# Performance work log

Measured on AMD Instinct MI355X. Metric: run time of the kernel, lower is better.

## Reference

```python
import jax, jax.numpy as jnp
import numpy as np

B, T, D = 4, 2048, 2048
K, D_B, TOPK, WINDOW = 7, 128, 16, 64
GATE_CAP = 1.0
STRAND_CAP = 1.0
_PHI = 1.618033988749895
_PSI = -0.6180339887498949


def _ln(x, g, b, eps=1e-5):
    m = jnp.mean(x, axis=-1, keepdims=True)
    v = jnp.mean((x - m) ** 2, axis=-1, keepdims=True)
    return (x - m) * jax.lax.rsqrt(v + eps) * g + b


def setup_inputs() -> dict:
    ks = jax.random.split(jax.random.key(0), 20)
    rn = lambda k, s, sc=1.0: jax.random.normal(k, s, jnp.float32) * sc
    d_s = 1.0 / np.sqrt(D)
    db_s = 1.0 / np.sqrt(D_B)
    return {
        'X_write': rn(ks[0], (B, T, D)),
        'X_read': rn(ks[1], (B, T, D)),
        'slots': rn(ks[2], (B, K, D_B)),
        'W0': rn(ks[3], (D, D), d_s),
        'ln_write_g': jnp.ones((D,), jnp.float32),
        'ln_write_b': jnp.zeros((D,), jnp.float32),
        'Wv': rn(ks[4], (D_B, D), d_s),
        'Wk': rn(ks[5], (D_B, D_B), db_s),
        'slot_key_bias': rn(ks[6], (K, D_B), 2.0),
        'Wg_w': rn(ks[7], (D_B, 2 * D_B), 1.0 / np.sqrt(2 * D_B)),
        'Wg_b': jnp.full((D_B,), -2.0, jnp.float32),
        'ln_strand_g': jnp.ones((D_B,), jnp.float32),
        'ln_strand_b': jnp.zeros((D_B,), jnp.float32),
        'Wsq': rn(ks[8], (D_B, D_B), db_s),
        'Wsk': rn(ks[9], (D_B, D_B), db_s),
        'Wsv': rn(ks[10], (D_B, D_B), db_s),
        'lambda_strand': rn(ks[11], (D_B,), 0.1),
        'Wq_read': rn(ks[12], (D_B, D), d_s),
        'Wk_read': rn(ks[13], (D_B, D_B), db_s),
        'Wv_read': rn(ks[14], (D, D_B), db_s),
        'render_coeffs': rn(ks[15], (K, 3, D), 0.1),
        'slot_temps': 1.0 + rn(ks[16], (K,), 0.1),
    }


def reference(X_write, X_read, slots, W0, ln_write_g, ln_write_b, Wv, Wk,
              slot_key_bias, Wg_w, Wg_b, ln_strand_g, ln_strand_b,
              Wsq, Wsk, Wsv, lambda_strand, Wq_read, Wk_read, Wv_read,
              render_coeffs, slot_temps):
    b, t, d = X_write.shape
    sd = 1.0 / np.sqrt(D_B)
    X_n = _ln(X_write, ln_write_g, ln_write_b)

    # --- banded salience + topk (torch.no_grad region; only int indices escape) ---
    W_eff = min(WINDOW, t - 1)
    Xs = jax.lax.stop_gradient(X_n)
    X_W0 = Xs @ jax.lax.stop_gradient(W0).T            # [b,t,d]
    Xp = jnp.pad(X_W0, ((0, 0), (W_eff, 0), (0, 0)))   # left-pad so offset w -> j = i + w - W

    def band_dot(w):
        return jnp.einsum('btd,btd->bt', Xs,
                          jax.lax.dynamic_slice_in_dim(Xp, w, t, axis=1))

    band = jax.vmap(band_dot)(jnp.arange(W_eff)).transpose(1, 2, 0)  # [b,t,W]
    ii = jnp.arange(t)[:, None]
    ww = jnp.arange(W_eff)[None, :]
    jj = ii + ww - W_eff
    valid = (jj >= 0) & (ii >= 1)                      # j in [max(0,i-W), i)
    sal = jnp.where(valid, band, -jnp.inf).reshape(b, -1)
    topk_eff = min(TOPK, t * (t - 1) // 2)
    _, idx = jax.lax.top_k(sal, topk_eff)              # [b,topk]
    i_idx = idx // W_eff
    j_idx = i_idx + (idx % W_eff) - W_eff

    # --- topk pair gather + bilinear relation ---
    x_new = jnp.take_along_axis(X_n, i_idx[..., None], axis=1)  # [b,topk,d]
    x_old = jnp.take_along_axis(X_n, j_idx[..., None], axis=1)
    pair_sal = jnp.sum(x_new * (x_old @ jax.lax.stop_gradient(W0).T), axis=-1)
    alpha = jax.nn.softmax(pair_sal, axis=-1)
    R_t = jnp.einsum('bp,bpe->be', alpha, (x_new - x_old) @ Wv.T)  # [b,d_b]

    # --- slot write ---
    slot_keys = slots @ Wk.T + slot_key_bias[None]
    compat = jnp.einsum('bke,be->bk', slot_keys, R_t) * sd
    compat = compat * jax.nn.softplus(slot_temps)[None]
    sw = jax.nn.softmax(compat, axis=-1)
    weighted_R = sw[..., None] * R_t[:, None, :]                 # [b,K,d_b]
    g = jax.nn.sigmoid(jnp.concatenate([slots, weighted_R], -1) @ Wg_w.T + Wg_b)
    slots_upd = (1.0 - g) * slots + g * weighted_R

    # --- strand mixer (KxK self-attention) ---
    B_ln = _ln(slots_upd, ln_strand_g, ln_strand_b)
    att = jax.nn.softmax(jnp.einsum('bke,bme->bkm', B_ln @ Wsq.T, B_ln @ Wsk.T) * sd, axis=-1)
    ctx = att @ (B_ln @ Wsv.T)
    slots_next = slots_upd + ctx * jnp.clip(jnp.tanh(lambda_strand), -STRAND_CAP, STRAND_CAP)

    # --- aux losses ---
    L_persist = jnp.mean((slots_next - slots) ** 2)
    nrm = jnp.linalg.norm(slots_next, axis=-1, keepdims=True)
    Bn = slots_next / jnp.maximum(nrm, 1e-12)
    cos = jnp.einsum('bke,bme->bkm', Bn, Bn)
    off = 1.0 - jnp.eye(K, dtype=cos.dtype)
    L_div = jnp.sum(cos ** 2 * off) / (b * K * (K - 1))

    # --- directional render gate + read ---
    q_r = X_read @ Wq_read.T                    # [b,t,d_b]
    k_r = slots_next @ Wk_read.T                # [b,K,d_b]
    v_r = slots_next @ Wv_read.T                # [b,K,d]
    scores = jnp.einsum('bte,bke->btk', q_r, k_r) * sd
    q_mean = jnp.mean(X_read, axis=1)           # [b,d]
    w0q = q_mean @ jax.lax.stop_gradient(W0).T
    dphi = _PHI - _PSI
    phi_q = (w0q - _PSI * q_mean) / dphi
    psi_q = (_PHI * q_mean - w0q) / dphi
    pm = jnp.linalg.norm(phi_q, axis=-1, keepdims=True)
    sm = jnp.linalg.norm(psi_q, axis=-1, keepdims=True)
    tot = pm + sm + 1e-6
    basis = jnp.concatenate([jnp.ones_like(pm), pm / tot, sm / tot], axis=-1)  # [b,3]
    gate = jnp.clip(jnp.tanh(jnp.einsum('bi,kid->bkd', basis, render_coeffs)),
                    -GATE_CAP, GATE_CAP)
    z = jnp.einsum('btk,bkd->btd', jax.nn.softmax(scores, axis=-1), v_r * gate)
    return z, slots_next, L_persist, L_div
```

## Files before the change

### kernel.cpp

```cpp
#include <hip/hip_runtime.h>
#include <cstdint>
#include <cstddef>

#define DEV __device__ __forceinline__

typedef __bf16 bf16x8 __attribute__((ext_vector_type(8)));
typedef float f32x4 __attribute__((ext_vector_type(4)));
typedef unsigned short u16;
typedef unsigned int u32;

constexpr int Bq = 4, Tq = 2048, Dq = 2048, Kq = 7, DB = 128, TK = 16;
constexpr float SD = 0.08838834764831845f;
constexpr float PHIc = 1.618033988749895f;
constexpr float PSIc = -0.6180339887498949f;
constexpr float DPHI = 2.2360679774997896f;
#define NEG_INF (-__builtin_inff())

DEV u16 f2bf(float f) {
  union { float f; u32 u; } x; x.f = f;
  u32 r = (x.u + 0x7fffu + ((x.u >> 16) & 1u)) >> 16;
  return (u16)r;
}
DEV float bfbits2f(u32 h) { union { u32 u; float f; } x; x.u = h << 16; return x.f; }

DEV void async16(void* l, const void* g) {
  __builtin_amdgcn_global_load_lds((const __attribute__((address_space(1))) void*)g,
                                   (__attribute__((address_space(3))) void*)l, 16, 0, 0);
}

__global__ __launch_bounds__(256) void k_w0b(const float* __restrict__ W0, u16* __restrict__ W0b) {
  size_t i = ((size_t)blockIdx.x * 256 + threadIdx.x) * 8;
  float4 a = *(const float4*)&W0[i];
  float4 c = *(const float4*)&W0[i + 4];
  u32 p0 = (u32)f2bf(a.x) | ((u32)f2bf(a.y) << 16);
  u32 p1 = (u32)f2bf(a.z) | ((u32)f2bf(a.w) << 16);
  u32 p2 = (u32)f2bf(c.x) | ((u32)f2bf(c.y) << 16);
  u32 p3 = (u32)f2bf(c.z) | ((u32)f2bf(c.w) << 16);
  uint4 st; st.x = p0; st.y = p1; st.z = p2; st.w = p3;
  *(uint4*)&W0b[i] = st;
}

__global__ __launch_bounds__(256) void k_ln(const float* __restrict__ X, const float* __restrict__ g,
                                            const float* __restrict__ bb, u16* __restrict__ Xn) {
  int row = blockIdx.x;
  const float* xr = X + (size_t)row * Dq;
  int tid = threadIdx.x, lane = tid & 63, w = tid >> 6;
  float4 a = *(const float4*)&xr[tid * 8];
  float4 c = *(const float4*)&xr[tid * 8 + 4];
  float s = a.x + a.y + a.z + a.w + c.x + c.y + c.z + c.w;
  float q = a.x*a.x + a.y*a.y + a.z*a.z + a.w*a.w + c.x*c.x + c.y*c.y + c.z*c.z + c.w*c.w;
  #pragma unroll
  for (int o = 32; o; o >>= 1) { s += __shfl_xor(s, o); q += __shfl_xor(q, o); }
  __shared__ float red[8];
  if (lane == 0) { red[w] = s; red[w + 4] = q; }
  __syncthreads();
  float S = red[0] + red[1] + red[2] + red[3];
  float Q = red[4] + red[5] + red[6] + red[7];
  float mean = S * (1.0f / Dq);
  float var = Q * (1.0f / Dq) - mean * mean;
  float rstd = rsqrtf(var + 1e-5f);
  float v[8] = {a.x, a.y, a.z, a.w, c.x, c.y, c.z, c.w};
  u32 p[4];
  #pragma unroll
  for (int j = 0; j < 4; ++j) {
    int d0 = tid * 8 + j * 2;
    float o0 = (v[j*2]   - mean) * rstd * g[d0]   + bb[d0];
    float o1 = (v[j*2+1] - mean) * rstd * g[d0+1] + bb[d0+1];
    p[j] = (u32)f2bf(o0) | ((u32)f2bf(o1) << 16);
  }
  uint4 st; st.x = p[0]; st.y = p[1]; st.z = p[2]; st.w = p[3];
  *(uint4*)&Xn[(size_t)row * Dq + tid * 8] = st;
}

__global__ __launch_bounds__(256) void k_qmean1(const float* __restrict__ X, float* __restrict__ part) {
  int s = blockIdx.x;
  int y = blockIdx.y;
  int b = blockIdx.z;
  int tid = threadIdx.x;
  const float* xb = X + (size_t)b * Tq * Dq + (size_t)s * 1024 + tid * 4;
  f32x4 acc = {0.f, 0.f, 0.f, 0.f};
  #pragma unroll 4
  for (int t = 0; t < 64; ++t) {
    const float4 v = *(const float4*)&xb[(size_t)(y * 64 + t) * Dq];
    acc[0] += v.x; acc[1] += v.y; acc[2] += v.z; acc[3] += v.w;
  }
  float4 st; st.x = acc[0]; st.y = acc[1]; st.z = acc[2]; st.w = acc[3];
  *(float4*)&part[((size_t)(b * 32 + y)) * Dq + s * 1024 + tid * 4] = st;
}

__global__ __launch_bounds__(256) void k_qmean2(const float* __restrict__ part, float* __restrict__ qm) {
  int s = blockIdx.x, b = blockIdx.y, tid = threadIdx.x;
  int col = s * 1024 + tid * 4;
  f32x4 acc = {0.f, 0.f, 0.f, 0.f};
  #pragma unroll 8
  for (int y = 0; y < 32; ++y) {
    float4 v = *(const float4*)&part[((size_t)(b * 32 + y)) * Dq + col];
    acc[0] += v.x; acc[1] += v.y; acc[2] += v.z; acc[3] += v.w;
  }
  float4 st;
  st.x = acc[0] * (1.0f / Tq); st.y = acc[1] * (1.0f / Tq);
  st.z = acc[2] * (1.0f / Tq); st.w = acc[3] * (1.0f / Tq);
  *(float4*)&qm[(size_t)b * Dq + col] = st;
}

__global__ __launch_bounds__(256) void k_w0q(const float* __restrict__ W0, const float* __restrict__ qm,
                                             float* __restrict__ w0q) {
  __shared__ float qs[4][Dq];
  int tid = threadIdx.x, lane = tid & 63, w = tid >> 6;
  for (int i = tid * 4; i < 4 * Dq; i += 1024) {
    *(float4*)&((float*)qs)[i] = *(const float4*)&qm[i];
  }
  __syncthreads();
  #pragma unroll
  for (int r = 0; r < 8; ++r) {
    int d = blockIdx.x * 32 + w * 8 + r;
    const float* wr = W0 + (size_t)d * Dq;
    float a0 = 0, a1 = 0, a2 = 0, a3 = 0;
    for (int e = lane * 4; e < Dq; e += 256) {
      float4 wv = *(const float4*)&wr[e];
      float4 q0 = *(const float4*)&qs[0][e];
      float4 q1 = *(const float4*)&qs[1][e];
      float4 q2 = *(const float4*)&qs[2][e];
      float4 q3 = *(const float4*)&qs[3][e];
      a0 += wv.x*q0.x + wv.y*q0.y + wv.z*q0.z + wv.w*q0.w;
      a1 += wv.x*q1.x + wv.y*q1.y + wv.z*q1.z + wv.w*q1.w;
      a2 += wv.x*q2.x + wv.y*q2.y + wv.z*q2.z + wv.w*q2.w;
      a3 += wv.x*q3.x + wv.y*q3.y + wv.z*q3.z + wv.w*q3.w;
    }
    #pragma unroll
    for (int o = 32; o; o >>= 1) {
      a0 += __shfl_xor(a0, o); a1 += __shfl_xor(a1, o);
      a2 += __shfl_xor(a2, o); a3 += __shfl_xor(a3, o);
    }
    if (lane == 0) {
      w0q[0 * Dq + d] = a0; w0q[1 * Dq + d] = a1;
      w0q[2 * Dq + d] = a2; w0q[3 * Dq + d] = a3;
    }
  }
}

__global__ __launch_bounds__(256) void k_basis(const float* __restrict__ qm, const float* __restrict__ w0q,
                                               float* __restrict__ basis) {
  int tid = threadIdx.x;
  __shared__ float red[256];
  __shared__ float psum;
  for (int b = 0; b < 4; ++b) {
    float ps = 0, ss = 0;
    for (int d = tid; d < Dq; d += 256) {
      float qv = qm[b * Dq + d], wv = w0q[b * Dq + d];
      float ph = (wv - PSIc * qv) * (1.0f / DPHI);
      float pv = (PHIc * qv - wv) * (1.0f / DPHI);
      ps += ph * ph; ss += pv * pv;
    }
    red[tid] = ps; __syncthreads();
    for (int st = 128; st; st >>= 1) { if (tid < st) red[tid] += red[tid + st]; __syncthreads(); }
    if (tid == 0) psum = red[0];
    __syncthreads();
    red[tid] = ss; __syncthreads();
    for (int st = 128; st; st >>= 1) { if (tid < st) red[tid] += red[tid + st]; __syncthreads(); }
    if (tid == 0) {
      float pm = sqrtf(psum), sm = sqrtf(red[0]);
      float tot = pm + sm + 1e-6f;
      basis[b * 3 + 0] = 1.0f; basis[b * 3 + 1] = pm / tot; basis[b * 3 + 2] = sm / tot;
    }
    __syncthreads();
  }
}

__global__ __launch_bounds__(256) void k_gemm(const u16* __restrict__ A, const u16* __restrict__ B,
                                              u16* __restrict__ C, int M, int N, int K) {
  __shared__ u16 As[128 * 64], Bs[128 * 64];
  int tid = threadIdx.x, lane = tid & 63, w = tid >> 6, wr = w >> 1, wc = w & 1;
  int bm = blockIdx.x, bn = blockIdx.y;
  const u16* Ab = A + (size_t)bm * 128 * K;
  const u16* Bb = B + (size_t)bn * 128 * K;
  f32x4 zero = {0.f, 0.f, 0.f, 0.f};
  f32x4 acc[4][4];
  #pragma unroll
  for (int mi = 0; mi < 4; ++mi)
    #pragma unroll
    for (int ni = 0; ni < 4; ++ni) acc[mi][ni] = zero;
  int ro = tid >> 3;
  int co = (tid & 7) * 8;
  int cs = co ^ ((ro & 7) * 8);
  for (int k0 = 0; k0 < K; k0 += 64) {
    #pragma unroll
    for (int i = 0; i < 4; ++i) {
      int row = ro + i * 32;
      async16(&As[row * 64 + co], Ab + (size_t)row * K + k0 + cs);
      async16(&Bs[row * 64 + co], Bb + (size_t)row * K + k0 + cs);
    }
    __syncthreads();
    #pragma unroll
    for (int ks = 0; ks < 2; ++ks) {
      int cbase = ks * 32 + ((lane >> 4) * 8);
      int crd = cbase ^ ((lane & 7) * 8);
      bf16x8 af[4], bfr[4];
      #pragma unroll
      for (int mi = 0; mi < 4; ++mi)
        af[mi] = *(const bf16x8*)&As[(wr * 64 + mi * 16 + (lane & 15)) * 64 + crd];
      #pragma unroll
      for (int ni = 0; ni < 4; ++ni)
        bfr[ni] = *(const bf16x8*)&Bs[(wc * 64 + ni * 16 + (lane & 15)) * 64 + crd];
      #pragma unroll
      for (int mi = 0; mi < 4; ++mi)
        #pragma unroll
        for (int ni = 0; ni < 4; ++ni)
          acc[mi][ni] = __builtin_amdgcn_mfma_f32_16x16x32_bf16(af[mi], bfr[ni], acc[mi][ni], 0, 0, 0);
    }
    __syncthreads();
  }
  int r0 = bm * 128 + wr * 64, c0 = bn * 128 + wc * 64;
  #pragma unroll
  for (int mi = 0; mi < 4; ++mi)
    #pragma unroll
    for (int ni = 0; ni < 4; ++ni) {
      int col = c0 + ni * 16 + (lane & 15);
      int rb = r0 + mi * 16 + ((lane >> 4) * 4);
      #pragma unroll
      for (int rg = 0; rg < 4; ++rg)
        C[(size_t)(rb + rg) * N + col] = f2bf(acc[mi][ni][rg]);
    }
}

__global__ __launch_bounds__(768) void k_band(const u16* __restrict__ Xn, const u16* __restrict__ XW0,
                                              float* __restrict__ sal) {
  int b = blockIdx.y, i0 = blockIdx.x * 32;
  int tid = threadIdx.x, lane = tid & 63, w = tid >> 6;
  int mi = w / 6, ni = w % 6;
  const u16* Xb = Xn + (size_t)b * Tq * Dq;
  const u16* Wb = XW0 + (size_t)b * Tq * Dq;
  int koff = (lane >> 4) * 8;
  const u16* ap = Xb + (size_t)(i0 + mi * 16 + (lane & 15)) * Dq + koff;
  int j = i0 - 64 + ni * 16 + (lane & 15); j = min(max(j, 0), Tq - 1);
  const u16* bp = Wb + (size_t)j * Dq + koff;
  f32x4 zero = {0.f, 0.f, 0.f, 0.f};
  f32x4 accA = zero, accB = zero;
  for (int k = 0; k < Dq; k += 64) {
    bf16x8 a0 = *(const bf16x8*)(ap + k);
    bf16x8 b0 = *(const bf16x8*)(bp + k);
    bf16x8 a1 = *(const bf16x8*)(ap + k + 32);
    bf16x8 b1 = *(const bf16x8*)(bp + k + 32);
    accA = __builtin_amdgcn_mfma_f32_16x16x32_bf16(a0, b0, accA, 0, 0, 0);
    accB = __builtin_amdgcn_mfma_f32_16x16x32_bf16(a1, b1, accB, 0, 0, 0);
  }
  int nl = ni * 16 + (lane & 15);
  #pragma unroll
  for (int rg = 0; rg < 4; ++rg) {
    int i = i0 + mi * 16 + (lane >> 4) * 4 + rg;
    int wb = nl - (i - i0);
    if (wb >= 0 && wb < 64) {
      int jj = i0 - 64 + nl;
      bool valid = (jj >= 0) && (i >= 1);
      sal[((size_t)b * Tq + i) * 64 + wb] = valid ? (accA[rg] + accB[rg]) : NEG_INF;
    }
  }
}

__global__ __launch_bounds__(256) void k_topk1(const float* __restrict__ sal,
                                               float* __restrict__ cv, int* __restrict__ ci) {
  int b = blockIdx.y, chunk = blockIdx.x;
  int tid = threadIdx.x, lane = tid & 63;
  const float* s = sal + (size_t)b * Tq * 64 + (size_t)chunk * 1024;
  float lv[4]; int li[4];
  #pragma unroll
  for (int i = 0; i < 4; ++i) { lv[i] = NEG_INF; li[i] = -1; }
  #pragma unroll
  for (int i = 0; i < 4; ++i) {
    int e = tid + i * 256;
    float v = s[e];
    int idx = chunk * 1024 + e;
    if (v > lv[3]) {
      lv[3] = v; li[3] = idx;
      #pragma unroll
      for (int q = 3; q > 0; --q)
        if (lv[q] > lv[q - 1]) {
          float tv = lv[q]; lv[q] = lv[q - 1]; lv[q - 1] = tv;
          int t2 = li[q]; li[q] = li[q - 1]; li[q - 1] = t2;
        }
    }
  }
  __shared__ float Sv[256][4];
  __shared__ int Si[256][4];
  __shared__ int heads[256];
  #pragma unroll
  for (int i = 0; i < 4; ++i) { Sv[tid][i] = lv[i]; Si[tid][i] = li[i]; }
  heads[tid] = 0;
  __syncthreads();
  float* ov = cv + ((size_t)b * 128 + chunk) * 16;
  int* oi = ci + ((size_t)b * 128 + chunk) * 16;
  for (int r = 0; r < 16; ++r) {
    if (tid < 64) {
      float best = NEG_INF; int bl = 0; int bidx = 0x7fffffff;
      #pragma unroll
      for (int cc = 0; cc < 4; ++cc) {
        int c = lane + cc * 64;
        int h = heads[c];
        float v = (h < 4) ? Sv[c][h] : NEG_INF;
        int ix = (h < 4) ? Si[c][h] : 0x7fffffff;
        if (v > best || (v == best && ix < bidx)) { best = v; bl = c; bidx = ix; }
      }
      #pragma unroll
      for (int o = 32; o; o >>= 1) {
        float bv = __shfl_xor(best, o); int blx = __shfl_xor(bl, o); int bix = __shfl_xor(bidx, o);
        if (bv > best || (bv == best && bix < bidx)) { best = bv; bl = blx; bidx = bix; }
      }
      if (lane == 0) {
        int h = heads[bl];
        ov[r] = best; oi[r] = (h < 4) ? Si[bl][h] : -1;
        heads[bl] = h + 1;
      }
    }
    __syncthreads();
  }
}

__global__ __launch_bounds__(256) void k_topk2(const float* __restrict__ cv, const int* __restrict__ ci,
                                               int* __restrict__ ti, int* __restrict__ tj) {
  int b = blockIdx.x, tid = threadIdx.x, lane = tid & 63;
  __shared__ float Sv[128][16];
  __shared__ int Si[128][16];
  __shared__ int heads[128];
  __shared__ int ridx[16];
  for (int i = tid; i < 128 * 16; i += 256) {
    ((float*)Sv)[i] = cv[(size_t)b * 2048 + i];
    ((int*)Si)[i] = ci[(size_t)b * 2048 + i];
  }
  if (tid < 128) heads[tid] = 0;
  __syncthreads();
  for (int r = 0; r < 16; ++r) {
    if (tid < 64) {
      float best = NEG_INF; int bl = 0; int bidx = 0x7fffffff;
      #pragma unroll
      for (int cc = 0; cc < 2; ++cc) {
        int c = lane + cc * 64;
        int h = heads[c];
        float v = (h < 16) ? Sv[c][h] : NEG_INF;
        int ix = (h < 16) ? Si[c][h] : 0x7fffffff;
        if (v > best || (v == best && ix < bidx)) { best = v; bl = c; bidx = ix; }
      }
      #pragma unroll
      for (int o = 32; o; o >>= 1) {
        float bv = __shfl_xor(best, o); int blx = __shfl_xor(bl, o); int bix = __shfl_xor(bidx, o);
        if (bv > best || (bv == best && bix < bidx)) { best = bv; bl = blx; bidx = bix; }
      }
      if (lane == 0) {
        int h = heads[bl];
        ridx[r] = Si[bl][h];
        heads[bl] = h + 1;
      }
    }
    __syncthreads();
  }
  if (tid < 16) {
    int fi = ridx[tid];
    int ii = fi >> 6;
    int jj = ii + (fi & 63) - 64;
    ti[b * TK + tid] = ii;
    tj[b * TK + tid] = jj;
  }
}

__global__ __launch_bounds__(256) void k_gatherln(const float* __restrict__ X, const float* __restrict__ g,
    const float* __restrict__ bb, const int* __restrict__ ti, const int* __restrict__ tj,
    float* __restrict__ Xnew, float* __restrict__ Xold) {
  int b = blockIdx.y, p = blockIdx.x >> 1, side = blockIdx.x & 1;
  int row = side ? tj[b * TK + p] : ti[b * TK + p];
  row = min(max(row, 0), Tq - 1);
  const float* xr = X + ((size_t)(b * Tq + row)) * Dq;
  float* dst = (side ? Xold : Xnew) + ((size_t)(b * TK + p)) * Dq;
  int tid = threadIdx.x, lane = tid & 63, w = tid >> 6;
  float4 a = *(const float4*)&xr[tid * 8];
  float4 c = *(const float4*)&xr[tid * 8 + 4];
  float s = a.x + a.y + a.z + a.w + c.x + c.y + c.z + c.w;
  float q = a.x*a.x + a.y*a.y + a.z*a.z + a.w*a.w + c.x*c.x + c.y*c.y + c.z*c.z + c.w*c.w;
  #pragma unroll
  for (int o = 32; o; o >>= 1) { s += __shfl_xor(s, o); q += __shfl_xor(q, o); }
  __shared__ float red[8];
  if (lane == 0) { red[w] = s; red[w + 4] = q; }
  __syncthreads();
  float S = red[0] + red[1] + red[2] + red[3];
  float Q = red[4] + red[5] + red[6] + red[7];
  float mean = S * (1.0f / Dq);
  float var = Q * (1.0f / Dq) - mean * mean;
  float rstd = rsqrtf(var + 1e-5f);
  float v[8] = {a.x, a.y, a.z, a.w, c.x, c.y, c.z, c.w};
  float o8[8];
  #pragma unroll
  for (int j = 0; j < 8; ++j) {
    int d = tid * 8 + j;
    o8[j] = (v[j] - mean) * rstd * g[d] + bb[d];
  }
  float4 s0; s0.x = o8[0]; s0.y = o8[1]; s0.z = o8[2]; s0.w = o8[3];
  float4 s1; s1.x = o8[4]; s1.y = o8[5]; s1.z = o8[6]; s1.w = o8[7];
  *(float4*)&dst[tid * 8] = s0;
  *(float4*)&dst[tid * 8 + 4] = s1;
}

__global__ __launch_bounds__(256) void k_pairsal(const float* __restrict__ W0, const float* __restrict__ Xnew,
                                                 const float* __restrict__ Xold, float* __restrict__ psal) {
  int d0 = blockIdx.x * 64, e0 = blockIdx.y * 64;
  int tid = threadIdx.x, P = tid & 63, dg = tid >> 6;
  f32x4 xo[16];
  #pragma unroll
  for (int i = 0; i < 16; ++i)
    xo[i] = *(const f32x4*)&Xold[(size_t)P * Dq + e0 + i * 4];
  int dbase = d0 + dg * 16;
  f32x4 xn[4];
  #pragma unroll
  for (int i = 0; i < 4; ++i)
    xn[i] = *(const f32x4*)&Xnew[(size_t)P * Dq + dbase + i * 4];
  float acc = 0.f;
  #pragma unroll
  for (int dd = 0; dd < 16; ++dd) {
    int d = __builtin_amdgcn_readfirstlane(dbase + dd);
    const float* wr = W0 + (size_t)d * Dq + e0;
    float i0 = 0.f, i1 = 0.f, i2 = 0.f, i3 = 0.f;
    #pragma unroll
    for (int i = 0; i < 16; ++i) {
      float4 wv = *(const float4*)&wr[i * 4];
      i0 += wv.x * xo[i][0]; i1 += wv.y * xo[i][1];
      i2 += wv.z * xo[i][2]; i3 += wv.w * xo[i][3];
    }
    acc += xn[dd >> 2][dd & 3] * ((i0 + i1) + (i2 + i3));
  }
  __shared__ float part[4][64];
  part[dg][P] = acc;
  __syncthreads();
  if (tid < 64)
    atomicAdd(&psal[tid], part[0][tid] + part[1][tid] + part[2][tid] + part[3][tid]);
}

__global__ __launch_bounds__(256) void k_alphart(const float* __restrict__ psal, const float* __restrict__ Xnew,
    const float* __restrict__ Xold, const float* __restrict__ Wv, float* __restrict__ Rt) {
  int bx = blockIdx.x, b = blockIdx.y;
  int tid = threadIdx.x, lane = tid & 63, w = tid >> 6;
  __shared__ float al[16], xd[Dq];
  if (tid == 0) {
    float mx = NEG_INF;
    #pragma unroll
    for (int p = 0; p < 16; ++p) mx = fmaxf(mx, psal[b * 16 + p]);
    float ee[16]; float s = 0.f;
    #pragma unroll
    for (int p = 0; p < 16; ++p) { ee[p] = expf(psal[b * 16 + p] - mx); s += ee[p]; }
    #pragma unroll
    for (int p = 0; p < 16; ++p) al[p] = ee[p] / s;
  }
  __syncthreads();
  {
    int d0 = tid * 8;
    float a8[8] = {0, 0, 0, 0, 0, 0, 0, 0};
    #pragma unroll
    for (int p = 0; p < 16; ++p) {
      const float* xn = Xnew + (size_t)(b * 16 + p) * Dq + d0;
      const float* xo = Xold + (size_t)(b * 16 + p) * Dq + d0;
      float ap = al[p];
      float4 n0 = *(const float4*)xn;
      float4 n1 = *(const float4*)(xn + 4);
      float4 o0 = *(const float4*)xo;
      float4 o1 = *(const float4*)(xo + 4);
      a8[0] += ap * (n0.x - o0.x); a8[1] += ap * (n0.y - o0.y);
      a8[2] += ap * (n0.z - o0.z); a8[3] += ap * (n0.w - o0.w);
      a8[4] += ap * (n1.x - o1.x); a8[5] += ap * (n1.y - o1.y);
      a8[6] += ap * (n1.z - o1.z); a8[7] += ap * (n1.w - o1.w);
    }
    #pragma unroll
    for (int j = 0; j < 8; ++j) xd[d0 + j] = a8[j];
  }
  __syncthreads();
  int e = bx * 4 + w;
  const float* wr = Wv + (size_t)e * Dq;
  float s = 0.f;
  #pragma unroll 8
  for (int d = lane; d < Dq; d += 64) s += wr[d] * xd[d];
  #pragma unroll
  for (int o = 32; o; o >>= 1) s += __shfl_xor(s, o);
  if (lane == 0) Rt[b * DB + e] = s;
}

__global__ __launch_bounds__(1024) void k_slots(
    const float* __restrict__ slots, const float* __restrict__ Wk, const float* __restrict__ skb,
    const float* __restrict__ Wgw, const float* __restrict__ Wgb,
    const float* __restrict__ lng, const float* __restrict__ lnb,
    const float* __restrict__ Wsq, const float* __restrict__ Wsk, const float* __restrict__ Wsv,
    const float* __restrict__ lam, const float* __restrict__ temps,
    const float* __restrict__ Rt, const float* __restrict__ Wkr,
    float* __restrict__ snOut, float* __restrict__ krOut) {
  int b = blockIdx.x, tid = threadIdx.x;
  int lane = tid & 63, w = tid >> 6;
  int sub = lane & 15, quad = lane >> 4;
  __shared__ float s_s[Kq][DB], r_s[DB], sk_s[Kq][DB], cm[8], sw[8],
                   su[Kq][DB], mv[Kq][2], bnl[Kq][DB],
                   qq[Kq][DB], kks[Kq][DB], vvs[Kq][DB],
                   att[Kq][8], sn_s[Kq][DB];
  for (int i = tid; i < Kq * DB; i += 1024) ((float*)s_s)[i] = slots[(size_t)b * Kq * DB + i];
  if (tid < DB) r_s[tid] = Rt[b * DB + tid];
  __syncthreads();
  #pragma unroll
  for (int r = 0; r < 14; ++r) {
    int idx = (w * 14 + r) * 4 + quad;
    int k = idx >> 7, e = idx & 127;
    const float* wr = Wk + e * DB;
    float a = 0.f;
    #pragma unroll
    for (int j = 0; j < 8; ++j) a += wr[sub + j * 16] * s_s[k][sub + j * 16];
    a += __shfl_xor(a, 8); a += __shfl_xor(a, 4); a += __shfl_xor(a, 2); a += __shfl_xor(a, 1);
    if (sub == 0) sk_s[k][e] = a + skb[idx];
  }
  __syncthreads();
  if (w < Kq) {
    float a = sk_s[w][lane] * r_s[lane] + sk_s[w][lane + 64] * r_s[lane + 64];
    #pragma unroll
    for (int o = 32; o; o >>= 1) a += __shfl_xor(a, o);
    if (lane == 0) {
      float t = temps[w];
      cm[w] = a * SD * log1pf(expf(t));
    }
  }
  __syncthreads();
  if (tid == 0) {
    float mx = cm[0];
    for (int k = 1; k < Kq; ++k) mx = fmaxf(mx, cm[k]);
    float ee[7]; float s = 0.f;
    for (int k = 0; k < Kq; ++k) { ee[k] = expf(cm[k] - mx); s += ee[k]; }
    for (int k = 0; k < Kq; ++k) sw[k] = ee[k] / s;
  }
  __syncthreads();
  #pragma unroll
  for (int r = 0; r < 14; ++r) {
    int idx = (w * 14 + r) * 4 + quad;
    int k = idx >> 7, e = idx & 127;
    const float* wr = Wgw + e * 256;
    float swk = sw[k];
    float a = 0.f;
    #pragma unroll
    for (int j = 0; j < 16; ++j) {
      int col = sub + j * 16;
      float x = (j < 8) ? s_s[k][col] : swk * r_s[col - 128];
      a += wr[col] * x;
    }
    a += __shfl_xor(a, 8); a += __shfl_xor(a, 4); a += __shfl_xor(a, 2); a += __shfl_xor(a, 1);
    if (sub == 0) {
      a += Wgb[e];
      float gv = 1.0f / (1.0f + expf(-a));
      float wrv = swk * r_s[e];
      su[k][e] = (1.0f - gv) * s_s[k][e] + gv * wrv;
    }
  }
  __syncthreads();
  if (w < Kq) {
    float v0 = su[w][lane], v1 = su[w][lane + 64];
    float s = v0 + v1, q = v0 * v0 + v1 * v1;
    #pragma unroll
    for (int o = 32; o; o >>= 1) { s += __shfl_xor(s, o); q += __shfl_xor(q, o); }
    if (lane == 0) {
      float m = s / DB; float va = q / DB - m * m;
      mv[w][0] = m; mv[w][1] = rsqrtf(va + 1e-5f);
    }
  }
  __syncthreads();
  for (int i = tid; i < Kq * DB; i += 1024) {
    int k = i >> 7, e = i & 127;
    bnl[k][e] = (su[k][e] - mv[k][0]) * mv[k][1] * lng[e] + lnb[e];
  }
  __syncthreads();
  #pragma unroll
  for (int r = 0; r < 14; ++r) {
    int idx = (w * 14 + r) * 4 + quad;
    int k = idx >> 7, e = idx & 127;
    const float* wr1 = Wsq + e * DB;
    const float* wr2 = Wsk + e * DB;
    const float* wr3 = Wsv + e * DB;
    float a1 = 0.f, a2 = 0.f, a3 = 0.f;
    #pragma unroll
    for (int j = 0; j < 8; ++j) {
      float x = bnl[k][sub + j * 16];
      a1 += wr1[sub + j * 16] * x;
      a2 += wr2[sub + j * 16] * x;
      a3 += wr3[sub + j * 16] * x;
    }
    #pragma unroll
    for (int o = 8; o; o >>= 1) {
      a1 += __shfl_xor(a1, o); a2 += __shfl_xor(a2, o); a3 += __shfl_xor(a3, o);
    }
    if (sub == 0) { qq[k][e] = a1; kks[k][e] = a2; vvs[k][e] = a3; }
  }
  __syncthreads();
  {
    int t4 = w * 4 + quad;
    if (t4 < 49) {
      int k = t4 / 7, m = t4 % 7;
      float a = 0.f;
      #pragma unroll
      for (int j = 0; j < 8; ++j) a += qq[k][sub + j * 16] * kks[m][sub + j * 16];
      a += __shfl_xor(a, 8); a += __shfl_xor(a, 4); a += __shfl_xor(a, 2); a += __shfl_xor(a, 1);
      if (sub == 0) att[k][m] = a * SD;
    }
  }
  __syncthreads();
  if (tid < Kq) {
    float mx = att[tid][0];
    for (int m = 1; m < Kq; ++m) mx = fmaxf(mx, att[tid][m]);
    float ee[7]; float s = 0.f;
    for (int m = 0; m < Kq; ++m) { ee[m] = expf(att[tid][m] - mx); s += ee[m]; }
    for (int m = 0; m < Kq; ++m) att[tid][m] = ee[m] / s;
  }
  __syncthreads();
  for (int i = tid; i < Kq * DB; i += 1024) {
    int k = i >> 7, e = i & 127;
    float c = 0.f;
    #pragma unroll
    for (int m = 0; m < Kq; ++m) c += att[k][m] * vvs[m][e];
    float l = tanhf(lam[e]); l = fminf(fmaxf(l, -1.0f), 1.0f);
    float v = su[k][e] + c * l;
    sn_s[k][e] = v;
    snOut[(size_t)b * Kq * DB + i] = v;
  }
  __syncthreads();
  #pragma unroll
  for (int r = 0; r < 14; ++r) {
    int idx = (w * 14 + r) * 4 + quad;
    int k = idx >> 7, e = idx & 127;
    const float* wr = Wkr + e * DB;
    float a = 0.f;
    #pragma unroll
    for (int j = 0; j < 8; ++j) a += wr[sub + j * 16] * sn_s[k][sub + j * 16];
    a += __shfl_xor(a, 8); a += __shfl_xor(a, 4); a += __shfl_xor(a, 2); a += __shfl_xor(a, 1);
    if (sub == 0) krOut[(size_t)b * Kq * DB + idx] = a;
  }
}

__global__ __launch_bounds__(256) void k_mvg(const float* __restrict__ snOut, const float* __restrict__ krOut,
    const float* __restrict__ Wqr, const float* __restrict__ Wvr, const float* __restrict__ rc,
    const float* __restrict__ basis, u16* __restrict__ Mb, u16* __restrict__ Vgb) {
  int b = blockIdx.y, tid = threadIdx.x;
  int d = blockIdx.x * 256 + tid;
  __shared__ float krs[Kq][DB], sns[Kq][DB];
  for (int i = tid; i < Kq * DB; i += 256) {
    ((float*)krs)[i] = krOut[(size_t)b * Kq * DB + i];
    ((float*)sns)[i] = snOut[(size_t)b * Kq * DB + i];
  }
  __syncthreads();
  float b0 = basis[b * 3 + 0], b1 = basis[b * 3 + 1], b2 = basis[b * 3 + 2];
  float am[7] = {0, 0, 0, 0, 0, 0, 0};
  for (int e = 0; e < DB; ++e) {
    float wq = Wqr[(size_t)e * Dq + d];
    #pragma unroll
    for (int k = 0; k < 7; ++k) am[k] += krs[k][e] * wq;
  }
  float vr[7] = {0, 0, 0, 0, 0, 0, 0};
  const float* wvrow = Wvr + (size_t)d * DB;
  for (int e = 0; e < DB; ++e) {
    float wv = wvrow[e];
    #pragma unroll
    for (int k = 0; k < 7; ++k) vr[k] += sns[k][e] * wv;
  }
  #pragma unroll
  for (int k = 0; k < 7; ++k) {
    Mb[((size_t)b * 7 + k) * Dq + d] = f2bf(am[k]);
    float gt = tanhf(b0 * rc[((size_t)k * 3 + 0) * Dq + d] +
                     b1 * rc[((size_t)k * 3 + 1) * Dq + d] +
                     b2 * rc[((size_t)k * 3 + 2) * Dq + d]);
    gt = fminf(fmaxf(gt, -1.0f), 1.0f);
    Vgb[((size_t)b * 7 + k) * Dq + d] = f2bf(vr[k] * gt);
  }
}

__global__ __launch_bounds__(256) void k_losses(const float* __restrict__ slots, const float* __restrict__ sn,
                                                float* __restrict__ out2) {
  int tid = threadIdx.x;
  __shared__ float red[256];
  __shared__ float nrm[28];
  float p = 0.f;
  for (int i = tid; i < Bq * Kq * DB; i += 256) { float d = sn[i] - slots[i]; p += d * d; }
  red[tid] = p; __syncthreads();
  for (int st = 128; st; st >>= 1) { if (tid < st) red[tid] += red[tid + st]; __syncthreads(); }
  if (tid == 0) out2[0] = red[0] / (float)(Bq * Kq * DB);
  if (tid < 28) {
    int b = tid / 7, k = tid % 7;
    float s = 0.f;
    for (int e = 0; e < DB; ++e) { float v = sn[(size_t)(b * 7 + k) * DB + e]; s += v * v; }
    nrm[tid] = fmaxf(sqrtf(s), 1e-12f);
  }
  __syncthreads();
  float dv = 0.f;
  if (tid < 168) {
    int b = tid / 42, r = tid % 42;
    int k = r / 6, m = r % 6; m += (m >= k);
    float dot = 0.f;
    for (int e = 0; e < DB; ++e)
      dot += sn[(size_t)(b * 7 + k) * DB + e] * sn[(size_t)(b * 7 + m) * DB + e];
    float c = dot / (nrm[b * 7 + k] * nrm[b * 7 + m]);
    dv = c * c;
  }
  red[tid] = dv; __syncthreads();
  for (int st = 128; st; st >>= 1) { if (tid < st) red[tid] += red[tid + st]; __syncthreads(); }
  if (tid == 0) out2[1] = red[0] / 168.0f;
}

__global__ __launch_bounds__(256) void k_z(const float* __restrict__ X, const u16* __restrict__ Mb,
                                           const u16* __restrict__ Vgb, float* __restrict__ Z) {
  int b = blockIdx.y, t0 = blockIdx.x * 16;
  int tid = threadIdx.x, lane = tid & 63, w = tid >> 6;
  __shared__ u16 Ms[7 * 2048], Vs[7 * 2048];
  for (int i = tid * 4; i < 7 * 2048; i += 1024) {
    *(uint2*)&Ms[i] = *(const uint2*)&Mb[(size_t)b * 7 * 2048 + i];
    *(uint2*)&Vs[i] = *(const uint2*)&Vgb[(size_t)b * 7 * 2048 + i];
  }
  __syncthreads();
  for (int ri = 0; ri < 4; ++ri) {
    int t = t0 + ri * 4 + w;
    const float* xr = X + ((size_t)b * Tq + t) * Dq;
    float sc[7] = {0, 0, 0, 0, 0, 0, 0};
    #pragma unroll
    for (int i = 0; i < 8; ++i) {
      int d = lane * 4 + i * 256;
      float4 x = *(const float4*)&xr[d];
      #pragma unroll
      for (int k = 0; k < 7; ++k) {
        uint2 mm = *(const uint2*)&Ms[k * 2048 + d];
        sc[k] += x.x * bfbits2f(mm.x & 0xffffu) + x.y * bfbits2f(mm.x >> 16)
               + x.z * bfbits2f(mm.y & 0xffffu) + x.w * bfbits2f(mm.y >> 16);
      }
    }
    #pragma unroll
    for (int k = 0; k < 7; ++k) {
      #pragma unroll
      for (int o = 32; o; o >>= 1) sc[k] += __shfl_xor(sc[k], o);
    }
    float mx = sc[0];
    #pragma unroll
    for (int k = 1; k < 7; ++k) mx = fmaxf(mx, sc[k]);
    float pz[7]; float s = 0.f;
    #pragma unroll
    for (int k = 0; k < 7; ++k) { pz[k] = expf((sc[k] - mx) * SD); s += pz[k]; }
    float inv = 1.0f / s;
    #pragma unroll
    for (int k = 0; k < 7; ++k) pz[k] *= inv;
    float* zr = Z + ((size_t)b * Tq + t) * Dq;
    #pragma unroll
    for (int i = 0; i < 8; ++i) {
      int d = lane * 4 + i * 256;
      float4 o4; o4.x = o4.y = o4.z = o4.w = 0.f;
      #pragma unroll
      for (int k = 0; k < 7; ++k) {
        uint2 vm = *(const uint2*)&Vs[k * 2048 + d];
        float pk = pz[k];
        o4.x += pk * bfbits2f(vm.x & 0xffffu); o4.y += pk * bfbits2f(vm.x >> 16);
        o4.z += pk * bfbits2f(vm.y & 0xffffu); o4.w += pk * bfbits2f(vm.y >> 16);
      }
      *(float4*)&zr[d] = o4;
    }
  }
}

extern "C" void kernel_launch(void* const* d_in, const int* in_sizes, int n_in,
                              void* d_out, int out_size, void* d_ws, size_t ws_size,
                              hipStream_t stream) {
  const float* Xw   = (const float*)d_in[0];
  const float* Xr   = (const float*)d_in[1];
  const float* slots= (const float*)d_in[2];
  const float* W0   = (const float*)d_in[3];
  const float* lng  = (const float*)d_in[4];
  const float* lnb  = (const float*)d_in[5];
  const float* Wv   = (const float*)d_in[6];
  const float* Wk   = (const float*)d_in[7];
  const float* skb  = (const float*)d_in[8];
  const float* Wgw  = (const float*)d_in[9];
  const float* Wgb  = (const float*)d_in[10];
  const float* lsg  = (const float*)d_in[11];
  const float* lsb  = (const float*)d_in[12];
  const float* Wsq  = (const float*)d_in[13];
  const float* Wsk  = (const float*)d_in[14];
  const float* Wsv  = (const float*)d_in[15];
  const float* lam  = (const float*)d_in[16];
  const float* Wqr  = (const float*)d_in[17];
  const float* Wkr  = (const float*)d_in[18];
  const float* Wvr  = (const float*)d_in[19];
  const float* rc   = (const float*)d_in[20];
  const float* temps= (const float*)d_in[21];

  char* wsb = (char*)d_ws;
  size_t off = 0;
  auto alloc = [&](size_t bytes) -> void* {
    void* p = wsb + off;
    off += (bytes + 255) & ~(size_t)255;
    return p;
  };
  u16*   Xn   = (u16*)  alloc((size_t)Bq * Tq * Dq * 2);
  u16*   XW0  = (u16*)  alloc((size_t)Bq * Tq * Dq * 2);
  u16*   W0b  = (u16*)  alloc((size_t)Dq * Dq * 2);
  float* sal  = (float*)alloc((size_t)Bq * Tq * 64 * 4);
  int*   ti   = (int*)  alloc(Bq * TK * 4);
  int*   tj   = (int*)  alloc(Bq * TK * 4);
  float* Xnew = (float*)alloc((size_t)Bq * TK * Dq * 4);
  float* Xold = (float*)alloc((size_t)Bq * TK * Dq * 4);
  float* psal = (float*)alloc(Bq * TK * 4);
  float* Rt   = (float*)alloc(Bq * DB * 4);
  float* qm   = (float*)alloc(Bq * Dq * 4);
  float* w0q  = (float*)alloc(Bq * Dq * 4);
  float* basis= (float*)alloc(Bq * 3 * 4);
  float* krOut= (float*)alloc(Bq * Kq * DB * 4);
  u16*   Mbf  = (u16*)  alloc((size_t)Bq * Kq * Dq * 2);
  u16*   Vgb  = (u16*)  alloc((size_t)Bq * Kq * Dq * 2);
  float* cv   = (float*)alloc((size_t)Bq * 128 * 16 * 4);
  int*   ci   = (int*)  alloc((size_t)Bq * 128 * 16 * 4);
  float* part = (float*)alloc((size_t)Bq * 32 * Dq * 4);

  float* Zout = (float*)d_out;
  float* snOut = Zout + (size_t)Bq * Tq * Dq;
  float* lossOut = snOut + Bq * Kq * DB;

  k_w0b   <<<2048, 256, 0, stream>>>(W0, W0b);
  k_ln    <<<Bq * Tq, 256, 0, stream>>>(Xw, lng, lnb, Xn);
  k_qmean1<<<dim3(2, 32, Bq), 256, 0, stream>>>(Xr, part);
  k_qmean2<<<dim3(2, Bq), 256, 0, stream>>>(part, qm);
  k_w0q   <<<64, 256, 0, stream>>>(W0, qm, w0q);
  k_basis <<<1, 256, 0, stream>>>(qm, w0q, basis);
  k_gemm  <<<dim3(64, 16), 256, 0, stream>>>(Xn, W0b, XW0, Bq * Tq, Dq, Dq);
  k_band  <<<dim3(64, Bq), 768, 0, stream>>>(Xn, XW0, sal);
  k_topk1 <<<dim3(128, Bq), 256, 0, stream>>>(sal, cv, ci);
  k_topk2 <<<Bq, 256, 0, stream>>>(cv, ci, ti, tj);
  k_gatherln<<<dim3(32, Bq), 256, 0, stream>>>(Xw, lng, lnb, ti, tj, Xnew, Xold);
  hipMemsetAsync(psal, 0, Bq * TK * 4, stream);
  k_pairsal<<<dim3(32, 32), 256, 0, stream>>>(W0, Xnew, Xold, psal);
  k_alphart<<<dim3(32, Bq), 256, 0, stream>>>(psal, Xnew, Xold, Wv, Rt);
  k_slots <<<Bq, 1024, 0, stream>>>(slots, Wk, skb, Wgw, Wgb, lsg, lsb, Wsq, Wsk, Wsv,
                                    lam, temps, Rt, Wkr, snOut, krOut);
  k_mvg   <<<dim3(8, Bq), 256, 0, stream>>>(snOut, krOut, Wqr, Wvr, rc, basis, Mbf, Vgb);
  k_losses<<<1, 256, 0, stream>>>(slots, snOut, lossOut);
  k_z     <<<dim3(128, Bq), 256, 0, stream>>>(Xr, Mbf, Vgb, Zout);
}
```

Baseline: 444.9 us.

## Split slot update into per-slot kernels and widen small reduction grids

Replaces the single per-batch 1024-thread slot-update kernel with four kernels gridded over (slot, batch), passing intermediates through global buffers so more CUs work on the tiny slot math. k_w0q is launched with 256 blocks of 2 rows per wave instead of 64 blocks, and k_basis runs one block per batch instead of looping over batches. k_z now reads the M/V tables directly from global memory instead of staging them in shared memory. These small kernels are latency-bound, so the extra launches and global round trips may cancel the parallelism gain, and dropping the LDS staging in k_z relies on cache hits.

```diff
diff --git a/kernel.cpp b/kernel.cpp
--- a/kernel.cpp
+++ b/kernel.cpp
@@ -73,9 +73,7 @@
 }
 
 __global__ __launch_bounds__(256) void k_qmean1(const float* __restrict__ X, float* __restrict__ part) {
-  int s = blockIdx.x;
-  int y = blockIdx.y;
-  int b = blockIdx.z;
+  int s = blockIdx.x, y = blockIdx.y, b = blockIdx.z;
   int tid = threadIdx.x;
   const float* xb = X + (size_t)b * Tq * Dq + (size_t)s * 1024 + tid * 4;
   f32x4 acc = {0.f, 0.f, 0.f, 0.f};
@@ -112,8 +110,8 @@
   }
   __syncthreads();
   #pragma unroll
-  for (int r = 0; r < 8; ++r) {
-    int d = blockIdx.x * 32 + w * 8 + r;
+  for (int r = 0; r < 2; ++r) {
+    int d = blockIdx.x * 8 + w * 2 + r;
     const float* wr = W0 + (size_t)d * Dq;
     float a0 = 0, a1 = 0, a2 = 0, a3 = 0;
     for (int e = lane * 4; e < Dq; e += 256) {
@@ -141,29 +139,26 @@
 
 __global__ __launch_bounds__(256) void k_basis(const float* __restrict__ qm, const float* __restrict__ w0q,
                                                float* __restrict__ basis) {
-  int tid = threadIdx.x;
+  int b = blockIdx.x, tid = threadIdx.x;
   __shared__ float red[256];
   __shared__ float psum;
-  for (int b = 0; b < 4; ++b) {
-    float ps = 0, ss = 0;
-    for (int d = tid; d < Dq; d += 256) {
-      float qv = qm[b * Dq + d], wv = w0q[b * Dq + d];
-      float ph = (wv - PSIc * qv) * (1.0f / DPHI);
-      float pv = (PHIc * qv - wv) * (1.0f / DPHI);
-      ps += ph * ph; ss += pv * pv;
-    }
-    red[tid] = ps; __syncthreads();
-    for (int st = 128; st; st >>= 1) { if (tid < st) red[tid] += red[tid + st]; __syncthreads(); }
-    if (tid == 0) psum = red[0];
-    __syncthreads();
-    red[tid] = ss; __syncthreads();
-    for (int st = 128; st; st >>= 1) { if (tid < st) red[tid] += red[tid + st]; __syncthreads(); }
-    if (tid == 0) {
-      float pm = sqrtf(psum), sm = sqrtf(red[0]);
-      float tot = pm + sm + 1e-6f;
-      basis[b * 3 + 0] = 1.0f; basis[b * 3 + 1] = pm / tot; basis[b * 3 + 2] = sm / tot;
-    }
-    __syncthreads();
+  float ps = 0, ss = 0;
+  for (int d = tid; d < Dq; d += 256) {
+    float qv = qm[b * Dq + d], wv = w0q[b * Dq + d];
+    float ph = (wv - PSIc * qv) * (1.0f / DPHI);
+    float pv = (PHIc * qv - wv) * (1.0f / DPHI);
+    ps += ph * ph; ss += pv * pv;
+  }
+  red[tid] = ps; __syncthreads();
+  for (int st = 128; st; st >>= 1) { if (tid < st) red[tid] += red[tid + st]; __syncthreads(); }
+  if (tid == 0) psum = red[0];
+  __syncthreads();
+  red[tid] = ss; __syncthreads();
+  for (int st = 128; st; st >>= 1) { if (tid < st) red[tid] += red[tid + st]; __syncthreads(); }
+  if (tid == 0) {
+    float pm = sqrtf(psum), sm = sqrtf(red[0]);
+    float tot = pm + sm + 1e-6f;
+    basis[b * 3 + 0] = 1.0f; basis[b * 3 + 1] = pm / tot; basis[b * 3 + 2] = sm / tot;
   }
 }
 
@@ -478,65 +473,70 @@
   if (lane == 0) Rt[b * DB + e] = s;
 }
 
-__global__ __launch_bounds__(1024) void k_slots(
-    const float* __restrict__ slots, const float* __restrict__ Wk, const float* __restrict__ skb,
-    const float* __restrict__ Wgw, const float* __restrict__ Wgb,
+__global__ __launch_bounds__(256) void ksl_a(const float* __restrict__ slots, const float* __restrict__ Wk,
+    const float* __restrict__ skb, const float* __restrict__ Rt, const float* __restrict__ temps,
+    float* __restrict__ compat) {
+  int k = blockIdx.x, b = blockIdx.y;
+  int tid = threadIdx.x, g = tid >> 4, sub = tid & 15;
+  __shared__ float s_s[DB], r_s[DB], sk_s[DB];
+  if (tid < DB) { s_s[tid] = slots[((size_t)(b * Kq + k)) * DB + tid]; r_s[tid] = Rt[b * DB + tid]; }
+  __syncthreads();
+  #pragma unroll
+  for (int r = 0; r < 8; ++r) {
+    int e = g * 8 + r;
+    const float* wr = Wk + e * DB;
+    float a = 0.f;
+    #pragma unroll
+    for (int j = 0; j < 8; ++j) a += wr[sub + j * 16] * s_s[sub + j * 16];
+    a += __shfl_xor(a, 8); a += __shfl_xor(a, 4); a += __shfl_xor(a, 2); a += __shfl_xor(a, 1);
+    if (sub == 0) sk_s[e] = a + skb[k * DB + e];
+  }
+  __syncthreads();
+  if (tid < 64) {
+    float a = sk_s[tid] * r_s[tid] + sk_s[tid + 64] * r_s[tid + 64];
+    #pragma unroll
+    for (int o = 32; o; o >>= 1) a += __shfl_xor(a, o);
+    if (tid == 0) {
+      float t = temps[k];
+      compat[b * Kq + k] = a * SD * log1pf(expf(t));
+    }
+  }
+}
+
+__global__ __launch_bounds__(64) void ksl_b(const float* __restrict__ compat, float* __restrict__ swg) {
+  int b = blockIdx.x;
+  if (threadIdx.x == 0) {
+    float cm[Kq];
+    float mx = NEG_INF;
+    for (int k = 0; k < Kq; ++k) { cm[k] = compat[b * Kq + k]; mx = fmaxf(mx, cm[k]); }
+    float s = 0.f;
+    for (int k = 0; k < Kq; ++k) { cm[k] = expf(cm[k] - mx); s += cm[k]; }
+    for (int k = 0; k < Kq; ++k) swg[b * Kq + k] = cm[k] / s;
+  }
+}
+
+__global__ __launch_bounds__(256) void ksl_c(const float* __restrict__ slots, const float* __restrict__ Rt,
+    const float* __restrict__ swg, const float* __restrict__ Wgw, const float* __restrict__ Wgb,
     const float* __restrict__ lng, const float* __restrict__ lnb,
     const float* __restrict__ Wsq, const float* __restrict__ Wsk, const float* __restrict__ Wsv,
-    const float* __restrict__ lam, const float* __restrict__ temps,
-    const float* __restrict__ Rt, const float* __restrict__ Wkr,
-    float* __restrict__ snOut, float* __restrict__ krOut) {
-  int b = blockIdx.x, tid = threadIdx.x;
-  int lane = tid & 63, w = tid >> 6;
-  int sub = lane & 15, quad = lane >> 4;
-  __shared__ float s_s[Kq][DB], r_s[DB], sk_s[Kq][DB], cm[8], sw[8],
-                   su[Kq][DB], mv[Kq][2], bnl[Kq][DB],
-                   qq[Kq][DB], kks[Kq][DB], vvs[Kq][DB],
-                   att[Kq][8], sn_s[Kq][DB];
-  for (int i = tid; i < Kq * DB; i += 1024) ((float*)s_s)[i] = slots[(size_t)b * Kq * DB + i];
-  if (tid < DB) r_s[tid] = Rt[b * DB + tid];
-  __syncthreads();
-  #pragma unroll
-  for (int r = 0; r < 14; ++r) {
-    int idx = (w * 14 + r) * 4 + quad;
-    int k = idx >> 7, e = idx & 127;
-    const float* wr = Wk + e * DB;
-    float a = 0.f;
-    #pragma unroll
-    for (int j = 0; j < 8; ++j) a += wr[sub + j * 16] * s_s[k][sub + j * 16];
-    a += __shfl_xor(a, 8); a += __shfl_xor(a, 4); a += __shfl_xor(a, 2); a += __shfl_xor(a, 1);
-    if (sub == 0) sk_s[k][e] = a + skb[idx];
-  }
-  __syncthreads();
-  if (w < Kq) {
-    float a = sk_s[w][lane] * r_s[lane] + sk_s[w][lane + 64] * r_s[lane + 64];
-    #pragma unroll
-    for (int o = 32; o; o >>= 1) a += __shfl_xor(a, o);
-    if (lane == 0) {
-      float t = temps[w];
-      cm[w] = a * SD * log1pf(expf(t));
-    }
-  }
-  __syncthreads();
-  if (tid == 0) {
-    float mx = cm[0];
-    for (int k = 1; k < Kq; ++k) mx = fmaxf(mx, cm[k]);
-    float ee[7]; float s = 0.f;
-    for (int k = 0; k < Kq; ++k) { ee[k] = expf(cm[k] - mx); s += ee[k]; }
-    for (int k = 0; k < Kq; ++k) sw[k] = ee[k] / s;
-  }
-  __syncthreads();
-  #pragma unroll
-  for (int r = 0; r < 14; ++r) {
-    int idx = (w * 14 + r) * 4 + quad;
-    int k = idx >> 7, e = idx & 127;
+    float* __restrict__ suOut, float* __restrict__ qqOut, float* __restrict__ kkOut,
+    float* __restrict__ vvOut) {
+  int k = blockIdx.x, b = blockIdx.y;
+  int tid = threadIdx.x, g = tid >> 4, sub = tid & 15;
+  __shared__ float s_s[DB], r_s[DB], su[DB], bnl[DB];
+  __shared__ float mvm, mvr;
+  if (tid < DB) { s_s[tid] = slots[((size_t)(b * Kq + k)) * DB + tid]; r_s[tid] = Rt[b * DB + tid]; }
+  __syncthreads();
+  float swk = swg[b * Kq + k];
+  #pragma unroll
+  for (int r = 0; r < 8; ++r) {
+    int e = g * 8 + r;
     const float* wr = Wgw + e * 256;
-    float swk = sw[k];
     float a = 0.f;
     #pragma unroll
     for (int j = 0; j < 16; ++j) {
       int col = sub + j * 16;
-      float x = (j < 8) ? s_s[k][col] : swk * r_s[col - 128];
+      float x = (j < 8) ? s_s[col] : swk * r_s[col - 128];
       a += wr[col] * x;
     }
     a += __shfl_xor(a, 8); a += __shfl_xor(a, 4); a += __shfl_xor(a, 2); a += __shfl_xor(a, 1);
@@ -544,37 +544,36 @@
       a += Wgb[e];
       float gv = 1.0f / (1.0f + expf(-a));
       float wrv = swk * r_s[e];
-      su[k][e] = (1.0f - gv) * s_s[k][e] + gv * wrv;
-    }
-  }
-  __syncthreads();
-  if (w < Kq) {
-    float v0 = su[w][lane], v1 = su[w][lane + 64];
+      su[e] = (1.0f - gv) * s_s[e] + gv * wrv;
+    }
+  }
+  __syncthreads();
+  if (tid < 64) {
+    float v0 = su[tid], v1 = su[tid + 64];
     float s = v0 + v1, q = v0 * v0 + v1 * v1;
     #pragma unroll
     for (int o = 32; o; o >>= 1) { s += __shfl_xor(s, o); q += __shfl_xor(q, o); }
-    if (lane == 0) {
+    if (tid == 0) {
       float m = s / DB; float va = q / DB - m * m;
-      mv[w][0] = m; mv[w][1] = rsqrtf(va + 1e-5f);
-    }
-  }
-  __syncthreads();
-  for (int i = tid; i < Kq * DB; i += 1024) {
-    int k = i >> 7, e = i & 127;
-    bnl[k][e] = (su[k][e] - mv[k][0]) * mv[k][1] * lng[e] + lnb[e];
-  }
-  __syncthreads();
-  #pragma unroll
-  for (int r = 0; r < 14; ++r) {
-    int idx = (w * 14 + r) * 4 + quad;
-    int k = idx >> 7, e = idx & 127;
+      mvm = m; mvr = rsqrtf(va + 1e-5f);
+    }
+  }
+  __syncthreads();
+  if (tid < DB) {
+    bnl[tid] = (su[tid] - mvm) * mvr * lng[tid] + lnb[tid];
+    suOut[((size_t)(b * Kq + k)) * DB + tid] = su[tid];
+  }
+  __syncthreads();
+  #pragma unroll
+  for (int r = 0; r < 8; ++r) {
+    int e = g * 8 + r;
     const float* wr1 = Wsq + e * DB;
     const float* wr2 = Wsk + e * DB;
     const float* wr3 = Wsv + e * DB;
     float a1 = 0.f, a2 = 0.f, a3 = 0.f;
     #pragma unroll
     for (int j = 0; j < 8; ++j) {
-      float x = bnl[k][sub + j * 16];
+      float x = bnl[sub + j * 16];
       a1 += wr1[sub + j * 16] * x;
       a2 += wr2[sub + j * 16] * x;
       a3 += wr3[sub + j * 16] * x;
@@ -583,50 +582,61 @@
     for (int o = 8; o; o >>= 1) {
       a1 += __shfl_xor(a1, o); a2 += __shfl_xor(a2, o); a3 += __shfl_xor(a3, o);
     }
-    if (sub == 0) { qq[k][e] = a1; kks[k][e] = a2; vvs[k][e] = a3; }
-  }
-  __syncthreads();
-  {
-    int t4 = w * 4 + quad;
-    if (t4 < 49) {
-      int k = t4 / 7, m = t4 % 7;
-      float a = 0.f;
-      #pragma unroll
-      for (int j = 0; j < 8; ++j) a += qq[k][sub + j * 16] * kks[m][sub + j * 16];
-      a += __shfl_xor(a, 8); a += __shfl_xor(a, 4); a += __shfl_xor(a, 2); a += __shfl_xor(a, 1);
-      if (sub == 0) att[k][m] = a * SD;
-    }
-  }
-  __syncthreads();
-  if (tid < Kq) {
-    float mx = att[tid][0];
-    for (int m = 1; m < Kq; ++m) mx = fmaxf(mx, att[tid][m]);
-    float ee[7]; float s = 0.f;
-    for (int m = 0; m < Kq; ++m) { ee[m] = expf(att[tid][m] - mx); s += ee[m]; }
-    for (int m = 0; m < Kq; ++m) att[tid][m] = ee[m] / s;
-  }
-  __syncthreads();
-  for (int i = tid; i < Kq * DB; i += 1024) {
-    int k = i >> 7, e = i & 127;
+    if (sub == 0) {
+      size_t oi = ((size_t)(b * Kq + k)) * DB + e;
+      qqOut[oi] = a1; kkOut[oi] = a2; vvOut[oi] = a3;
+    }
+  }
+}
+
+__global__ __launch_bounds__(256) void ksl_d(const float* __restrict__ suOut, const float* __restrict__ qqOut,
+    const float* __restrict__ kkOut, const float* __restrict__ vvOut, const float* __restrict__ lam,
+    const float* __restrict__ Wkr, float* __restrict__ snOut, float* __restrict__ krOut) {
+  int k = blockIdx.x, b = blockIdx.y;
+  int tid = threadIdx.x, g = tid >> 4, sub = tid & 15;
+  __shared__ float qq[DB], kks[Kq][DB], vvs[Kq][DB], att[8], sn_s[DB];
+  if (tid < DB) qq[tid] = qqOut[((size_t)(b * Kq + k)) * DB + tid];
+  for (int i = tid; i < Kq * DB; i += 256) {
+    ((float*)kks)[i] = kkOut[(size_t)b * Kq * DB + i];
+    ((float*)vvs)[i] = vvOut[(size_t)b * Kq * DB + i];
+  }
+  __syncthreads();
+  if (tid < 112) {
+    int m = g;
+    float a = 0.f;
+    #pragma unroll
+    for (int j = 0; j < 8; ++j) a += qq[sub + j * 16] * kks[m][sub + j * 16];
+    a += __shfl_xor(a, 8); a += __shfl_xor(a, 4); a += __shfl_xor(a, 2); a += __shfl_xor(a, 1);
+    if (sub == 0) att[m] = a * SD;
+  }
+  __syncthreads();
+  if (tid == 0) {
+    float mx = att[0];
+    for (int m = 1; m < Kq; ++m) mx = fmaxf(mx, att[m]);
+    float s = 0.f;
+    for (int m = 0; m < Kq; ++m) { att[m] = expf(att[m] - mx); s += att[m]; }
+    for (int m = 0; m < Kq; ++m) att[m] /= s;
+  }
+  __syncthreads();
+  if (tid < DB) {
     float c = 0.f;
     #pragma unroll
-    for (int m = 0; m < Kq; ++m) c += att[k][m] * vvs[m][e];
-    float l = tanhf(lam[e]); l = fminf(fmaxf(l, -1.0f), 1.0f);
-    float v = su[k][e] + c * l;
-    sn_s[k][e] = v;
-    snOut[(size_t)b * Kq * DB + i] = v;
-  }
-  __syncthreads();
-  #pragma unroll
-  for (int r = 0; r < 14; ++r) {
-    int idx = (w * 14 + r) * 4 + quad;
-    int k = idx >> 7, e = idx & 127;
+    for (int m = 0; m < Kq; ++m) c += att[m] * vvs[m][tid];
+    float l = tanhf(lam[tid]); l = fminf(fmaxf(l, -1.0f), 1.0f);
+    float v = suOut[((size_t)(b * Kq + k)) * DB + tid] + c * l;
+    sn_s[tid] = v;
+    snOut[((size_t)(b * Kq + k)) * DB + tid] = v;
+  }
+  __syncthreads();
+  #pragma unroll
+  for (int r = 0; r < 8; ++r) {
+    int e = g * 8 + r;
     const float* wr = Wkr + e * DB;
     float a = 0.f;
     #pragma unroll
-    for (int j = 0; j < 8; ++j) a += wr[sub + j * 16] * sn_s[k][sub + j * 16];
+    for (int j = 0; j < 8; ++j) a += wr[sub + j * 16] * sn_s[sub + j * 16];
     a += __shfl_xor(a, 8); a += __shfl_xor(a, 4); a += __shfl_xor(a, 2); a += __shfl_xor(a, 1);
-    if (sub == 0) krOut[(size_t)b * Kq * DB + idx] = a;
+    if (sub == 0) krOut[((size_t)(b * Kq + k)) * DB + e] = a;
   }
 }
 
@@ -702,12 +712,8 @@
                                            const u16* __restrict__ Vgb, float* __restrict__ Z) {
   int b = blockIdx.y, t0 = blockIdx.x * 16;
   int tid = threadIdx.x, lane = tid & 63, w = tid >> 6;
-  __shared__ u16 Ms[7 * 2048], Vs[7 * 2048];
-  for (int i = tid * 4; i < 7 * 2048; i += 1024) {
-    *(uint2*)&Ms[i] = *(const uint2*)&Mb[(size_t)b * 7 * 2048 + i];
-    *(uint2*)&Vs[i] = *(const uint2*)&Vgb[(size_t)b * 7 * 2048 + i];
-  }
-  __syncthreads();
+  const u16* Ms = Mb + (size_t)b * 7 * 2048;
+  const u16* Vs = Vgb + (size_t)b * 7 * 2048;
   for (int ri = 0; ri < 4; ++ri) {
     int t = t0 + ri * 4 + w;
     const float* xr = X + ((size_t)b * Tq + t) * Dq;
@@ -806,6 +812,12 @@
   float* cv   = (float*)alloc((size_t)Bq * 128 * 16 * 4);
   int*   ci   = (int*)  alloc((size_t)Bq * 128 * 16 * 4);
   float* part = (float*)alloc((size_t)Bq * 32 * Dq * 4);
+  float* compat = (float*)alloc(Bq * Kq * 4);
+  float* swg  = (float*)alloc(Bq * Kq * 4);
+  float* suB  = (float*)alloc(Bq * Kq * DB * 4);
+  float* qqB  = (float*)alloc(Bq * Kq * DB * 4);
+  float* kkB  = (float*)alloc(Bq * Kq * DB * 4);
+  float* vvB  = (float*)alloc(Bq * Kq * DB * 4);
 
   float* Zout = (float*)d_out;
   float* snOut = Zout + (size_t)Bq * Tq * Dq;
@@ -815,8 +827,8 @@
   k_ln    <<<Bq * Tq, 256, 0, stream>>>(Xw, lng, lnb, Xn);
   k_qmean1<<<dim3(2, 32, Bq), 256, 0, stream>>>(Xr, part);
   k_qmean2<<<dim3(2, Bq), 256, 0, stream>>>(part, qm);
-  k_w0q   <<<64, 256, 0, stream>>>(W0, qm, w0q);
-  k_basis <<<1, 256, 0, stream>>>(qm, w0q, basis);
+  k_w0q   <<<256, 256, 0, stream>>>(W0, qm, w0q);
+  k_basis <<<Bq, 256, 0, stream>>>(qm, w0q, basis);
   k_gemm  <<<dim3(64, 16), 256, 0, stream>>>(Xn, W0b, XW0, Bq * Tq, Dq, Dq);
   k_band  <<<dim3(64, Bq), 768, 0, stream>>>(Xn, XW0, sal);
   k_topk1 <<<dim3(128, Bq), 256, 0, stream>>>(sal, cv, ci);
@@ -825,8 +837,11 @@
   hipMemsetAsync(psal, 0, Bq * TK * 4, stream);
   k_pairsal<<<dim3(32, 32), 256, 0, stream>>>(W0, Xnew, Xold, psal);
   k_alphart<<<dim3(32, Bq), 256, 0, stream>>>(psal, Xnew, Xold, Wv, Rt);
-  k_slots <<<Bq, 1024, 0, stream>>>(slots, Wk, skb, Wgw, Wgb, lsg, lsb, Wsq, Wsk, Wsv,
-                                    lam, temps, Rt, Wkr, snOut, krOut);
+  ksl_a   <<<dim3(Kq, Bq), 256, 0, stream>>>(slots, Wk, skb, Rt, temps, compat);
+  ksl_b   <<<Bq, 64, 0, stream>>>(compat, swg);
+  ksl_c   <<<dim3(Kq, Bq), 256, 0, stream>>>(slots, Rt, swg, Wgw, Wgb, lsg, lsb,
+                                             Wsq, Wsk, Wsv, suB, qqB, kkB, vvB);
+  ksl_d   <<<dim3(Kq, Bq), 256, 0, stream>>>(suB, qqB, kkB, vvB, lam, Wkr, snOut, krOut);
   k_mvg   <<<dim3(8, Bq), 256, 0, stream>>>(snOut, krOut, Wqr, Wvr, rc, basis, Mbf, Vgb);
   k_losses<<<1, 256, 0, stream>>>(slots, snOut, lossOut);
   k_z     <<<dim3(128, Bq), 256, 0, stream>>>(Xr, Mbf, Vgb, Zout);
```

Result: faster. 422.1 us (-5.1%).
